# Performance work log

Measured on AMD Instinct MI355X. Metric: run time of the kernel, lower is better.

## Reference

```python
import jax, jax.numpy as jnp
import numpy as np

BN_EPS = 1e-5


def setup_inputs() -> dict:
    key = jax.random.key(0)
    ks = jax.random.split(key, 3)
    B, S, C, H, W = 4, 8, 64, 96, 96
    P = 6
    DIM = 768
    x = jax.random.normal(ks[0], (B, S, C, H, W), dtype=jnp.float32)
    conv_w = jax.random.normal(ks[1], (C, C, 3, 3), dtype=jnp.float32) * 0.05
    conv_b = jnp.zeros((C,), dtype=jnp.float32)
    bn_gamma = jnp.ones((C,), dtype=jnp.float32)
    bn_beta = jnp.zeros((C,), dtype=jnp.float32)
    bn_mean = jnp.zeros((C,), dtype=jnp.float32)
    bn_var = jnp.ones((C,), dtype=jnp.float32)
    proj_w = jax.random.normal(ks[2], (DIM, P * P * C), dtype=jnp.float32) * 0.02
    proj_b = jnp.zeros((DIM,), dtype=jnp.float32)
    mask = jnp.ones((P, P), dtype=jnp.float32)
    return {"x": x, "conv_w": conv_w, "conv_b": conv_b,
            "bn_gamma": bn_gamma, "bn_beta": bn_beta,
            "bn_mean": bn_mean, "bn_var": bn_var,
            "proj_w": proj_w, "proj_b": proj_b,
            "mask": mask, "patch_size": P}


def reference(x, conv_w, conv_b, bn_gamma, bn_beta, bn_mean, bn_var,
              proj_w, proj_b, mask, patch_size):
    B, S, C, H, W = x.shape
    p = patch_size
    Cout = conv_w.shape[0]
    # Fuse the per-frame loop: run conv over all B*S frames at once.
    xf = x.reshape(B * S, C, H, W)
    y = jax.lax.conv_general_dilated(
        xf, conv_w, window_strides=(1, 1), padding=[(1, 1), (1, 1)],
        dimension_numbers=("NCHW", "OIHW", "NCHW"))
    y = y + conv_b[None, :, None, None]
    # BatchNorm2d (eval-mode running stats); Dropout2d is identity at eval.
    inv = jax.lax.rsqrt(bn_var + BN_EPS)
    y = (y - bn_mean[None, :, None, None]) * (bn_gamma * inv)[None, :, None, None] \
        + bn_beta[None, :, None, None]
    y = jax.nn.gelu(y, approximate=False)  # torch GELU default = exact erf
    y = y.reshape(B, S, Cout, H, W)
    # Patch extraction, row-major over (l_idx, r_idx) exactly as the loop.
    pr = H // p  # patches per row
    patches = y.reshape(B, S, Cout, pr, p, pr, p).transpose(0, 1, 3, 5, 2, 4, 6)
    patches = patches.reshape(B, S, pr * pr, Cout, p, p) * mask  # [B,S,P,C,p,p]
    # Flatten(start_dim=2 on [B,S,C,p,p]) + Linear + GELU, batched over patches.
    flat = patches.reshape(B, S, pr * pr, Cout * p * p)
    tokens = jax.nn.gelu(
        jnp.einsum("bsnf,df->bsnd", flat, proj_w) + proj_b, approximate=False)
    return tokens, patches
```

## Files before the change

### kernel.cpp

```cpp
#include <hip/hip_runtime.h>
#include <hip/hip_bf16.h>
#include <math.h>


typedef unsigned short u16;
typedef __bf16 bf16x8 __attribute__((ext_vector_type(8)));
typedef float f32x4 __attribute__((ext_vector_type(4)));

#define NFRM 32
#define CH 64
#define HW 96
#define HWP 98
#define KP 2304
#define DIMN 768
#define MTOK 8192
#define TOKN (MTOK * DIMN)
#define NPAT (MTOK * KP)
#define XHWC_ELEMS ((size_t)NFRM * HWP * HWP * CH)
#define BP_OFF XHWC_ELEMS
#define PW_OFF (BP_OFF + 36864)
#define BSTR 200

static __device__ __forceinline__ u16 f2b(float f) {
  unsigned u = __builtin_bit_cast(unsigned, f);
  u += 0x7fffu + ((u >> 16) & 1u);
  return (u16)(u >> 16);
}
static __device__ __forceinline__ float gelu_f(float x) {
  return 0.5f * x * (1.0f + erff(x * 0.7071067811865476f));
}

typedef __attribute__((address_space(3))) unsigned int lds_uint;
typedef __attribute__((address_space(1))) const unsigned int g_uint;
static __device__ __forceinline__ void gload16(const u16* g, u16* s) {
  __builtin_amdgcn_global_load_lds((g_uint*)g, (lds_uint*)s, 16, 0, 0);
}

__global__ __launch_bounds__(256) void k_transpose(const float* __restrict__ x,
                                                   u16* __restrict__ xhwc) {
  __shared__ u16 tile[96 * 66];
  const int f = blockIdx.x / 96, h = blockIdx.x % 96;
  const int t = threadIdx.x;
  const float* xp = x + (size_t)f * CH * HW * HW + (size_t)h * HW;
#pragma unroll
  for (int k = 0; k < 6; ++k) {
    int e = (k * 256 + t) * 4;
    int ci = e / 96, w = e % 96;
    float4 v = *(const float4*)(xp + (size_t)ci * (HW * HW) + w);
    tile[(w + 0) * 66 + ci] = f2b(v.x);
    tile[(w + 1) * 66 + ci] = f2b(v.y);
    tile[(w + 2) * 66 + ci] = f2b(v.z);
    tile[(w + 3) * 66 + ci] = f2b(v.w);
  }
  __syncthreads();
  u16* op = xhwc + ((size_t)(f * HWP + h + 1) * HWP + 1) * CH;
#pragma unroll
  for (int k = 0; k < 12; ++k) {
    int e2 = (k * 256 + t) * 2;
    int w = e2 >> 6, ci = e2 & 63;
    *(unsigned*)(op + e2) = *(const unsigned*)(&tile[w * 66 + ci]);
  }
}

__global__ __launch_bounds__(256) void k_bpack(const float* __restrict__ w,
                                               u16* __restrict__ bp) {
  int e = blockIdx.x * 256 + threadIdx.x;
  int co = e / 576, r = e - co * 576, tap = r >> 6, ci = r & 63;
  bp[e] = f2b(w[(co * 64 + ci) * 9 + tap]);
}

__global__ __launch_bounds__(256) void k_pw(const float* __restrict__ pw,
                                            u16* __restrict__ dst) {
  int e = (blockIdx.x * 256 + threadIdx.x) * 4;
  float4 v = *(const float4*)(pw + e);
  ushort4 o;
  o.x = f2b(v.x); o.y = f2b(v.y); o.z = f2b(v.z); o.w = f2b(v.w);
  *(ushort4*)(dst + e) = o;
}

__global__ __launch_bounds__(256, 2) void k_conv(
    const u16* __restrict__ xhwc, const u16* __restrict__ bw,
    const float* __restrict__ cb, const float* __restrict__ gma,
    const float* __restrict__ bta, const float* __restrict__ mu,
    const float* __restrict__ var, const float* __restrict__ msk,
    float* __restrict__ pout) {
  __shared__ alignas(16) char SMEM[76800];
  u16* Asm = (u16*)SMEM;
  u16* Bsm = (u16*)(SMEM + 51200);
  float* Fsm = (float*)SMEM;

  const int bx = blockIdx.x;
  const int f = bx >> 5, rem = bx & 31, pr = rem >> 1, half = rem & 1;
  const int t = threadIdx.x, wv = t >> 6, l = t & 63, quad = l >> 4, lm = l & 15;
  const int wm = wv >> 1, wn = wv & 1;

  const u16* sbase = xhwc + (((size_t)f * HWP + pr * 6) * HWP + half * 48) * CH;
  const int pc = l >> 3;
  const int gsw = (l & 7) ^ pc;
  for (int c = wv; c < 50; c += 4) {
    const int p = c * 8 + pc;
    const int row = p / 50, ac = p - row * 50;
    gload16(sbase + ((size_t)row * HWP + ac) * CH + gsw * 8, Asm + c * 512);
  }

  int pb[9];
#pragma unroll
  for (int mf = 0; mf < 9; ++mf) {
    const int i16 = wm * 9 + mf;
    pb[mf] = (i16 / 3) * 50 + (i16 % 3) * 16 + lm;
  }
  f32x4 acc[9][2];
#pragma unroll
  for (int mf = 0; mf < 9; ++mf) {
    acc[mf][0] = (f32x4){0.f, 0.f, 0.f, 0.f};
    acc[mf][1] = (f32x4){0.f, 0.f, 0.f, 0.f};
  }

#pragma unroll
  for (int ph = 0; ph < 3; ++ph) {
    if (ph > 0) __syncthreads();
    for (int e = t; e < 1536; e += 256) {
      const int co = e / 24, kk = e - co * 24;
      *(uint4*)&Bsm[co * BSTR + kk * 8] =
          *(const uint4*)&bw[co * 576 + ph * 192 + kk * 8];
    }
    __syncthreads();
#pragma unroll
    for (int tp = 0; tp < 3; ++tp) {
      const int di = ph, dj = tp;
#pragma unroll
      for (int ks = 0; ks < 2; ++ks) {
        const int kq = ks * 4 + quad;
        const bf16x8 b0 = *(const bf16x8*)&Bsm[(wn * 32 + lm) * BSTR + tp * 64 + ks * 32 + quad * 8];
        const bf16x8 b1 = *(const bf16x8*)&Bsm[(wn * 32 + 16 + lm) * BSTR + tp * 64 + ks * 32 + quad * 8];
#pragma unroll
        for (int mf = 0; mf < 9; ++mf) {
          const int p = pb[mf] + di * 50 + dj;
          const bf16x8 a = *(const bf16x8*)&Asm[p * 64 + ((kq ^ (p & 7)) << 3)];
          acc[mf][0] = __builtin_amdgcn_mfma_f32_16x16x32_bf16(a, b0, acc[mf][0], 0, 0, 0);
          acc[mf][1] = __builtin_amdgcn_mfma_f32_16x16x32_bf16(a, b1, acc[mf][1], 0, 0, 0);
        }
      }
    }
  }

  __syncthreads();
#pragma unroll
  for (int nf = 0; nf < 2; ++nf) {
    const int co = wn * 32 + nf * 16 + lm;
    const float scv = gma[co] * rsqrtf(var[co] + 1e-5f);
    const float b2v = (cb[co] - mu[co]) * scv + bta[co];
#pragma unroll
    for (int mf = 0; mf < 9; ++mf) {
#pragma unroll
      for (int rg = 0; rg < 4; ++rg) {
        const int sp = wm * 144 + mf * 16 + quad * 4 + rg;
        const int orow = sp / 48, oc = sp - orow * 48;
        const int nl = oc / 6, pj = oc - nl * 6;
        const int jj = orow * 6 + pj;
        float v = acc[mf][nf][rg] * scv + b2v;
        v = gelu_f(v) * msk[jj];
        Fsm[nl * 2304 + co * 36 + jj] = v;
      }
    }
  }
  __syncthreads();
  float* pbase = pout + (size_t)(f * 256 + pr * 16 + half * 8) * KP;
#pragma unroll
  for (int k = 0; k < 18; ++k) {
    const int li = t + k * 256;
    *(float4*)&pbase[li * 4] = *(const float4*)&Fsm[li * 4];
  }
}

__global__ __launch_bounds__(256) void k_cvt(const float* __restrict__ pat,
                                             u16* __restrict__ abf) {
  int e = (blockIdx.x * 256 + threadIdx.x) * 4;
  float4 v = *(const float4*)(pat + e);
  ushort4 o;
  o.x = f2b(v.x); o.y = f2b(v.y); o.z = f2b(v.z); o.w = f2b(v.w);
  *(ushort4*)(abf + e) = o;
}

__global__ __launch_bounds__(256) void k_gemm(const u16* __restrict__ A,
                                              const u16* __restrict__ Bt,
                                              const float* __restrict__ pb,
                                              float* __restrict__ out) {
  __shared__ alignas(16) u16 As[128 * 64];
  __shared__ alignas(16) u16 Bs[64 * 64];
  const int bn = blockIdx.x % 12, bm = blockIdx.x / 12;
  const int m0 = bm * 128, n0 = bn * 64;
  const int t = threadIdx.x, wv = t >> 6, l = t & 63, quad = l >> 4, lm = l & 15;
  const int pc = l >> 3;
  const int gsw = (l & 7) ^ pc;

  f32x4 acc[2][4];
#pragma unroll
  for (int s = 0; s < 2; ++s)
#pragma unroll
    for (int u = 0; u < 4; ++u) acc[s][u] = (f32x4){0.f, 0.f, 0.f, 0.f};

  for (int k0 = 0; k0 < KP; k0 += 64) {
    __syncthreads();
    for (int c = wv; c < 24; c += 4) {
      if (c < 16) {
        const int row = c * 8 + pc;
        gload16(A + (size_t)(m0 + row) * KP + k0 + gsw * 8, As + c * 512);
      } else {
        const int row = (c - 16) * 8 + pc;
        gload16(Bt + (size_t)(n0 + row) * KP + k0 + gsw * 8, Bs + (c - 16) * 512);
      }
    }
    __syncthreads();
#pragma unroll
    for (int ks = 0; ks < 2; ++ks) {
      const int gx = ((ks * 4 + quad) ^ (lm & 7)) << 3;
      const bf16x8 a0 = *(const bf16x8*)&As[(wv * 32 + lm) * 64 + gx];
      const bf16x8 a1 = *(const bf16x8*)&As[(wv * 32 + 16 + lm) * 64 + gx];
#pragma unroll
      for (int u = 0; u < 4; ++u) {
        const bf16x8 b = *(const bf16x8*)&Bs[(u * 16 + lm) * 64 + gx];
        acc[0][u] = __builtin_amdgcn_mfma_f32_16x16x32_bf16(a0, b, acc[0][u], 0, 0, 0);
        acc[1][u] = __builtin_amdgcn_mfma_f32_16x16x32_bf16(a1, b, acc[1][u], 0, 0, 0);
      }
    }
  }
#pragma unroll
  for (int u = 0; u < 4; ++u) {
    const int n = n0 + u * 16 + lm;
    const float bias = pb[n];
#pragma unroll
    for (int s = 0; s < 2; ++s) {
#pragma unroll
      for (int rg = 0; rg < 4; ++rg) {
        const int m = m0 + wv * 32 + s * 16 + quad * 4 + rg;
        out[(size_t)m * DIMN + n] = gelu_f(acc[s][u][rg] + bias);
      }
    }
  }
}

extern "C" void kernel_launch(void* const* d_in, const int* in_sizes, int n_in,
                              void* d_out, int out_size, void* d_ws, size_t ws_size,
                              hipStream_t stream) {
  const float* x = (const float*)d_in[0];
  const float* conv_w = (const float*)d_in[1];
  const float* conv_b = (const float*)d_in[2];
  const float* bn_gamma = (const float*)d_in[3];
  const float* bn_beta = (const float*)d_in[4];
  const float* bn_mean = (const float*)d_in[5];
  const float* bn_var = (const float*)d_in[6];
  const float* proj_w = (const float*)d_in[7];
  const float* proj_b = (const float*)d_in[8];
  const float* mask = (const float*)d_in[9];
  float* out = (float*)d_out;
  float* patches = out + TOKN;
  u16* ws = (u16*)d_ws;
  u16* xhwc = ws;
  u16* bp = ws + BP_OFF;
  u16* pw = ws + PW_OFF;

  hipMemsetAsync(d_ws, 0, XHWC_ELEMS * sizeof(u16), stream);
  k_transpose<<<NFRM * HW, 256, 0, stream>>>(x, xhwc);
  k_bpack<<<144, 256, 0, stream>>>(conv_w, bp);
  k_pw<<<1728, 256, 0, stream>>>(proj_w, pw);
  k_conv<<<NFRM * 32, 256, 0, stream>>>(xhwc, bp, conv_b, bn_gamma, bn_beta,
                                        bn_mean, bn_var, mask, patches);
  k_cvt<<<18432, 256, 0, stream>>>(patches, xhwc);
  k_gemm<<<64 * 12, 256, 0, stream>>>(xhwc, pw, proj_b, out);
}
```

Before: 320.4 us.

## Fuse bf16 conversion into conv epilogue, stream weights from registers, widen GEMM K-tile

The conv kernel now writes a bf16 copy of the patches alongside the fp32 output, which removes the separate conversion pass over the large patch tensor whenever the workspace is large enough. Conv weights are read straight from global memory into registers with one-tap-ahead prefetch instead of being staged through LDS. That shrinks LDS enough to allow three blocks per CU, and the epilogue is split into two passes. A small halo-zeroing kernel replaces the full workspace memset, and both kernels remap block IDs for locality. The GEMM K-tile grows from 64 to 128 with a 16-way swizzle, halving the number of sync rounds while doubling LDS use.

```diff
diff --git a/kernel.cpp b/kernel.cpp
--- a/kernel.cpp
+++ b/kernel.cpp
@@ -19,7 +19,8 @@
 #define XHWC_ELEMS ((size_t)NFRM * HWP * HWP * CH)
 #define BP_OFF XHWC_ELEMS
 #define PW_OFF (BP_OFF + 36864)
-#define BSTR 200
+#define ABF_OFF (PW_OFF + 1769472)
+#define WS_NEED_FUSED (((size_t)ABF_OFF + (size_t)NPAT) * 2)
 
 static __device__ __forceinline__ u16 f2b(float f) {
   unsigned u = __builtin_bit_cast(unsigned, f);
@@ -34,6 +35,19 @@
 typedef __attribute__((address_space(1))) const unsigned int g_uint;
 static __device__ __forceinline__ void gload16(const u16* g, u16* s) {
   __builtin_amdgcn_global_load_lds((g_uint*)g, (lds_uint*)s, 16, 0, 0);
+}
+
+__global__ __launch_bounds__(256) void k_halo(u16* __restrict__ xhwc) {
+  const int e = blockIdx.x * 256 + threadIdx.x;
+  const int g = e & 7;
+  const int rest = e >> 3;
+  const int p = rest % 388, f = rest / 388;
+  int r, c;
+  if (p < 98)       { r = 0;       c = p; }
+  else if (p < 196) { r = 97;      c = p - 98; }
+  else if (p < 292) { r = p - 195; c = 0; }
+  else              { r = p - 291; c = 97; }
+  *(uint4*)&xhwc[(((size_t)f * HWP + r) * HWP + c) * CH + g * 8] = (uint4){0, 0, 0, 0};
 }
 
 __global__ __launch_bounds__(256) void k_transpose(const float* __restrict__ x,
@@ -78,19 +92,19 @@
   *(ushort4*)(dst + e) = o;
 }
 
-__global__ __launch_bounds__(256, 2) void k_conv(
+__global__ __launch_bounds__(256, 3) void k_conv(
     const u16* __restrict__ xhwc, const u16* __restrict__ bw,
     const float* __restrict__ cb, const float* __restrict__ gma,
     const float* __restrict__ bta, const float* __restrict__ mu,
     const float* __restrict__ var, const float* __restrict__ msk,
-    float* __restrict__ pout) {
-  __shared__ alignas(16) char SMEM[76800];
+    float* __restrict__ pout, u16* __restrict__ abf) {
+  __shared__ alignas(16) char SMEM[51200];
   u16* Asm = (u16*)SMEM;
-  u16* Bsm = (u16*)(SMEM + 51200);
   float* Fsm = (float*)SMEM;
 
-  const int bx = blockIdx.x;
-  const int f = bx >> 5, rem = bx & 31, pr = rem >> 1, half = rem & 1;
+  const int bid = blockIdx.x;
+  const int logical = (bid & 7) * 128 + (bid >> 3);
+  const int f = logical >> 5, rem = logical & 31, pr = rem >> 1, half = rem & 1;
   const int t = threadIdx.x, wv = t >> 6, l = t & 63, quad = l >> 4, lm = l & 15;
   const int wm = wv >> 1, wn = wv & 1;
 
@@ -116,35 +130,41 @@
     acc[mf][1] = (f32x4){0.f, 0.f, 0.f, 0.f};
   }
 
-#pragma unroll
-  for (int ph = 0; ph < 3; ++ph) {
-    if (ph > 0) __syncthreads();
-    for (int e = t; e < 1536; e += 256) {
-      const int co = e / 24, kk = e - co * 24;
-      *(uint4*)&Bsm[co * BSTR + kk * 8] =
-          *(const uint4*)&bw[co * 576 + ph * 192 + kk * 8];
-    }
-    __syncthreads();
-#pragma unroll
-    for (int tp = 0; tp < 3; ++tp) {
-      const int di = ph, dj = tp;
+  const u16* b0p = bw + (wn * 32 + lm) * 576 + quad * 8;
+  const u16* b1p = bw + (wn * 32 + 16 + lm) * 576 + quad * 8;
+  bf16x8 bc0[2], bc1[2], bn0[2], bn1[2];
+#pragma unroll
+  for (int ks = 0; ks < 2; ++ks) {
+    bc0[ks] = *(const bf16x8*)(b0p + ks * 32);
+    bc1[ks] = *(const bf16x8*)(b1p + ks * 32);
+  }
+  __syncthreads();
+
+#pragma unroll
+  for (int tap = 0; tap < 9; ++tap) {
+    const int di = tap / 3, dj = tap - di * 3;
+    if (tap < 8) {
 #pragma unroll
       for (int ks = 0; ks < 2; ++ks) {
-        const int kq = ks * 4 + quad;
-        const bf16x8 b0 = *(const bf16x8*)&Bsm[(wn * 32 + lm) * BSTR + tp * 64 + ks * 32 + quad * 8];
-        const bf16x8 b1 = *(const bf16x8*)&Bsm[(wn * 32 + 16 + lm) * BSTR + tp * 64 + ks * 32 + quad * 8];
-#pragma unroll
-        for (int mf = 0; mf < 9; ++mf) {
-          const int p = pb[mf] + di * 50 + dj;
-          const bf16x8 a = *(const bf16x8*)&Asm[p * 64 + ((kq ^ (p & 7)) << 3)];
-          acc[mf][0] = __builtin_amdgcn_mfma_f32_16x16x32_bf16(a, b0, acc[mf][0], 0, 0, 0);
-          acc[mf][1] = __builtin_amdgcn_mfma_f32_16x16x32_bf16(a, b1, acc[mf][1], 0, 0, 0);
-        }
-      }
-    }
-  }
-
-  __syncthreads();
+        bn0[ks] = *(const bf16x8*)(b0p + (tap + 1) * 64 + ks * 32);
+        bn1[ks] = *(const bf16x8*)(b1p + (tap + 1) * 64 + ks * 32);
+      }
+    }
+#pragma unroll
+    for (int ks = 0; ks < 2; ++ks) {
+      const int kq = ks * 4 + quad;
+#pragma unroll
+      for (int mf = 0; mf < 9; ++mf) {
+        const int p = pb[mf] + di * 50 + dj;
+        const bf16x8 a = *(const bf16x8*)&Asm[p * 64 + ((kq ^ (p & 7)) << 3)];
+        acc[mf][0] = __builtin_amdgcn_mfma_f32_16x16x32_bf16(a, bc0[ks], acc[mf][0], 0, 0, 0);
+        acc[mf][1] = __builtin_amdgcn_mfma_f32_16x16x32_bf16(a, bc1[ks], acc[mf][1], 0, 0, 0);
+      }
+    }
+#pragma unroll
+    for (int ks = 0; ks < 2; ++ks) { bc0[ks] = bn0[ks]; bc1[ks] = bn1[ks]; }
+  }
+
 #pragma unroll
   for (int nf = 0; nf < 2; ++nf) {
     const int co = wn * 32 + nf * 16 + lm;
@@ -152,24 +172,51 @@
     const float b2v = (cb[co] - mu[co]) * scv + bta[co];
 #pragma unroll
     for (int mf = 0; mf < 9; ++mf) {
+      const int orow = wm * 3 + mf / 3;
 #pragma unroll
       for (int rg = 0; rg < 4; ++rg) {
-        const int sp = wm * 144 + mf * 16 + quad * 4 + rg;
-        const int orow = sp / 48, oc = sp - orow * 48;
+        const int oc = (mf % 3) * 16 + quad * 4 + rg;
         const int nl = oc / 6, pj = oc - nl * 6;
         const int jj = orow * 6 + pj;
         float v = acc[mf][nf][rg] * scv + b2v;
-        v = gelu_f(v) * msk[jj];
-        Fsm[nl * 2304 + co * 36 + jj] = v;
+        acc[mf][nf][rg] = gelu_f(v) * msk[jj];
       }
     }
   }
   __syncthreads();
-  float* pbase = pout + (size_t)(f * 256 + pr * 16 + half * 8) * KP;
-#pragma unroll
-  for (int k = 0; k < 18; ++k) {
-    const int li = t + k * 256;
-    *(float4*)&pbase[li * 4] = *(const float4*)&Fsm[li * 4];
+#pragma unroll
+  for (int pass = 0; pass < 2; ++pass) {
+    if (pass) __syncthreads();
+#pragma unroll
+    for (int nf = 0; nf < 2; ++nf) {
+      const int co = wn * 32 + nf * 16 + lm;
+#pragma unroll
+      for (int mf = 0; mf < 9; ++mf) {
+        const int orow = wm * 3 + mf / 3;
+#pragma unroll
+        for (int rg = 0; rg < 4; ++rg) {
+          const int oc = (mf % 3) * 16 + quad * 4 + rg;
+          const int nl = oc / 6, pj = oc - nl * 6;
+          const int jj = orow * 6 + pj;
+          if ((nl >> 2) == pass)
+            Fsm[(nl & 3) * KP + co * 36 + jj] = acc[mf][nf][rg];
+        }
+      }
+    }
+    __syncthreads();
+    const size_t brow = (size_t)(f * 256 + pr * 16 + half * 8 + pass * 4) * KP;
+    float* pdst = pout + brow;
+#pragma unroll
+    for (int k = 0; k < 9; ++k) {
+      const int li = t + k * 256;
+      const float4 w = ((const float4*)Fsm)[li];
+      ((float4*)pdst)[li] = w;
+      if (abf) {
+        ushort4 o;
+        o.x = f2b(w.x); o.y = f2b(w.y); o.z = f2b(w.z); o.w = f2b(w.w);
+        *(ushort4*)&abf[brow + li * 4] = o;
+      }
+    }
   }
 }
 
@@ -186,13 +233,15 @@
                                               const u16* __restrict__ Bt,
                                               const float* __restrict__ pb,
                                               float* __restrict__ out) {
-  __shared__ alignas(16) u16 As[128 * 64];
-  __shared__ alignas(16) u16 Bs[64 * 64];
-  const int bn = blockIdx.x % 12, bm = blockIdx.x / 12;
+  __shared__ alignas(16) u16 As[128 * 128];
+  __shared__ alignas(16) u16 Bs[64 * 128];
+  const int bid = blockIdx.x;
+  const int logical = (bid & 7) * 96 + (bid >> 3);
+  const int bn = logical % 12, bm = logical / 12;
   const int m0 = bm * 128, n0 = bn * 64;
   const int t = threadIdx.x, wv = t >> 6, l = t & 63, quad = l >> 4, lm = l & 15;
-  const int pc = l >> 3;
-  const int gsw = (l & 7) ^ pc;
+  const int rl = l >> 4;
+  const int slot = l & 15;
 
   f32x4 acc[2][4];
 #pragma unroll
@@ -200,26 +249,28 @@
 #pragma unroll
     for (int u = 0; u < 4; ++u) acc[s][u] = (f32x4){0.f, 0.f, 0.f, 0.f};
 
-  for (int k0 = 0; k0 < KP; k0 += 64) {
+  for (int k0 = 0; k0 < KP; k0 += 128) {
     __syncthreads();
-    for (int c = wv; c < 24; c += 4) {
-      if (c < 16) {
-        const int row = c * 8 + pc;
+    for (int c = wv; c < 48; c += 4) {
+      if (c < 32) {
+        const int row = c * 4 + rl;
+        const int gsw = slot ^ (row & 15);
         gload16(A + (size_t)(m0 + row) * KP + k0 + gsw * 8, As + c * 512);
       } else {
-        const int row = (c - 16) * 8 + pc;
-        gload16(Bt + (size_t)(n0 + row) * KP + k0 + gsw * 8, Bs + (c - 16) * 512);
+        const int row = (c - 32) * 4 + rl;
+        const int gsw = slot ^ (row & 15);
+        gload16(Bt + (size_t)(n0 + row) * KP + k0 + gsw * 8, Bs + (c - 32) * 512);
       }
     }
     __syncthreads();
 #pragma unroll
-    for (int ks = 0; ks < 2; ++ks) {
-      const int gx = ((ks * 4 + quad) ^ (lm & 7)) << 3;
-      const bf16x8 a0 = *(const bf16x8*)&As[(wv * 32 + lm) * 64 + gx];
-      const bf16x8 a1 = *(const bf16x8*)&As[(wv * 32 + 16 + lm) * 64 + gx];
+    for (int ks = 0; ks < 4; ++ks) {
+      const int gx = ((ks * 4 + quad) ^ lm) << 3;
+      const bf16x8 a0 = *(const bf16x8*)&As[(wv * 32 + lm) * 128 + gx];
+      const bf16x8 a1 = *(const bf16x8*)&As[(wv * 32 + 16 + lm) * 128 + gx];
 #pragma unroll
       for (int u = 0; u < 4; ++u) {
-        const bf16x8 b = *(const bf16x8*)&Bs[(u * 16 + lm) * 64 + gx];
+        const bf16x8 b = *(const bf16x8*)&Bs[(u * 16 + lm) * 128 + gx];
         acc[0][u] = __builtin_amdgcn_mfma_f32_16x16x32_bf16(a0, b, acc[0][u], 0, 0, 0);
         acc[1][u] = __builtin_amdgcn_mfma_f32_16x16x32_bf16(a1, b, acc[1][u], 0, 0, 0);
       }
@@ -260,12 +311,18 @@
   u16* bp = ws + BP_OFF;
   u16* pw = ws + PW_OFF;
 
-  hipMemsetAsync(d_ws, 0, XHWC_ELEMS * sizeof(u16), stream);
+  const bool fused = ws_size >= WS_NEED_FUSED;
+  u16* abf = fused ? ws + ABF_OFF : (u16*)nullptr;
+
+  k_halo<<<388, 256, 0, stream>>>(xhwc);
   k_transpose<<<NFRM * HW, 256, 0, stream>>>(x, xhwc);
   k_bpack<<<144, 256, 0, stream>>>(conv_w, bp);
   k_pw<<<1728, 256, 0, stream>>>(proj_w, pw);
   k_conv<<<NFRM * 32, 256, 0, stream>>>(xhwc, bp, conv_b, bn_gamma, bn_beta,
-                                        bn_mean, bn_var, mask, patches);
-  k_cvt<<<18432, 256, 0, stream>>>(patches, xhwc);
-  k_gemm<<<64 * 12, 256, 0, stream>>>(xhwc, pw, proj_b, out);
-}
+                                        bn_mean, bn_var, mask, patches, abf);
+  if (!fused) {
+    k_cvt<<<18432, 256, 0, stream>>>(patches, xhwc);
+    abf = xhwc;
+  }
+  k_gemm<<<64 * 12, 256, 0, stream>>>(abf, pw, proj_b, out);
+}
```

Result: slower. 353.3 us (+10.3%).

## Fuse bf16 patch conversion into conv, zero only halo, rework GEMM staging

Applied to the files above, without the earlier changes.

The conv epilogue now also writes the bf16 copy of the patches into a dedicated workspace region when the workspace is large enough. This removes the separate fp32-to-bf16 conversion pass and its re-read of the patches tensor. The full-workspace memset is replaced by a small kernel that zeroes only the padding border of the HWC input. Separately, the projection GEMM switches from 64-wide async LDS loads with XOR swizzle to 32-wide K tiles loaded through registers into padded LDS rows. That doubles the number of barrier-synchronised iterations and drops the direct global-to-LDS path.

```diff
diff --git a/kernel.cpp b/kernel.cpp
--- a/kernel.cpp
+++ b/kernel.cpp
@@ -19,6 +19,8 @@
 #define XHWC_ELEMS ((size_t)NFRM * HWP * HWP * CH)
 #define BP_OFF XHWC_ELEMS
 #define PW_OFF (BP_OFF + 36864)
+#define ABF_OFF (PW_OFF + 1769472)
+#define WS_NEED_FUSED (((size_t)ABF_OFF + (size_t)NPAT) * 2)
 #define BSTR 200
 
 static __device__ __forceinline__ u16 f2b(float f) {
@@ -34,6 +36,19 @@
 typedef __attribute__((address_space(1))) const unsigned int g_uint;
 static __device__ __forceinline__ void gload16(const u16* g, u16* s) {
   __builtin_amdgcn_global_load_lds((g_uint*)g, (lds_uint*)s, 16, 0, 0);
+}
+
+__global__ __launch_bounds__(256) void k_halo(u16* __restrict__ xhwc) {
+  const int e = blockIdx.x * 256 + threadIdx.x;
+  const int g = e & 7;
+  const int rest = e >> 3;
+  const int p = rest % 388, f = rest / 388;
+  int r, c;
+  if (p < 98)       { r = 0;       c = p; }
+  else if (p < 196) { r = 97;      c = p - 98; }
+  else if (p < 292) { r = p - 195; c = 0; }
+  else              { r = p - 291; c = 97; }
+  *(uint4*)&xhwc[(((size_t)f * HWP + r) * HWP + c) * CH + g * 8] = (uint4){0, 0, 0, 0};
 }
 
 __global__ __launch_bounds__(256) void k_transpose(const float* __restrict__ x,
@@ -83,7 +98,7 @@
     const float* __restrict__ cb, const float* __restrict__ gma,
     const float* __restrict__ bta, const float* __restrict__ mu,
     const float* __restrict__ var, const float* __restrict__ msk,
-    float* __restrict__ pout) {
+    float* __restrict__ pout, u16* __restrict__ abf) {
   __shared__ alignas(16) char SMEM[76800];
   u16* Asm = (u16*)SMEM;
   u16* Bsm = (u16*)(SMEM + 51200);
@@ -165,11 +180,18 @@
     }
   }
   __syncthreads();
-  float* pbase = pout + (size_t)(f * 256 + pr * 16 + half * 8) * KP;
+  const size_t brow = (size_t)(f * 256 + pr * 16 + half * 8) * KP;
+  float* pbase = pout + brow;
 #pragma unroll
   for (int k = 0; k < 18; ++k) {
     const int li = t + k * 256;
-    *(float4*)&pbase[li * 4] = *(const float4*)&Fsm[li * 4];
+    const float4 w = *(const float4*)&Fsm[li * 4];
+    *(float4*)&pbase[li * 4] = w;
+    if (abf) {
+      ushort4 o;
+      o.x = f2b(w.x); o.y = f2b(w.y); o.z = f2b(w.z); o.w = f2b(w.w);
+      *(ushort4*)&abf[brow + li * 4] = o;
+    }
   }
 }
 
@@ -186,13 +208,12 @@
                                               const u16* __restrict__ Bt,
                                               const float* __restrict__ pb,
                                               float* __restrict__ out) {
-  __shared__ alignas(16) u16 As[128 * 64];
-  __shared__ alignas(16) u16 Bs[64 * 64];
+  __shared__ u16 As[128 * 40];
+  __shared__ u16 Bs[64 * 40];
   const int bn = blockIdx.x % 12, bm = blockIdx.x / 12;
   const int m0 = bm * 128, n0 = bn * 64;
   const int t = threadIdx.x, wv = t >> 6, l = t & 63, quad = l >> 4, lm = l & 15;
-  const int pc = l >> 3;
-  const int gsw = (l & 7) ^ pc;
+  const int ar = t >> 2, ac = (t & 3) * 8;
 
   f32x4 acc[2][4];
 #pragma unroll
@@ -200,29 +221,21 @@
 #pragma unroll
     for (int u = 0; u < 4; ++u) acc[s][u] = (f32x4){0.f, 0.f, 0.f, 0.f};
 
-  for (int k0 = 0; k0 < KP; k0 += 64) {
+  for (int k0 = 0; k0 < KP; k0 += 32) {
     __syncthreads();
-    for (int c = wv; c < 24; c += 4) {
-      if (c < 16) {
-        const int row = c * 8 + pc;
-        gload16(A + (size_t)(m0 + row) * KP + k0 + gsw * 8, As + c * 512);
-      } else {
-        const int row = (c - 16) * 8 + pc;
-        gload16(Bt + (size_t)(n0 + row) * KP + k0 + gsw * 8, Bs + (c - 16) * 512);
-      }
-    }
+    *(uint4*)&As[ar * 40 + ac] = *(const uint4*)&A[(size_t)(m0 + ar) * KP + k0 + ac];
+    *(uint4*)&As[(ar + 64) * 40 + ac] =
+        *(const uint4*)&A[(size_t)(m0 + ar + 64) * KP + k0 + ac];
+    *(uint4*)&Bs[ar * 40 + ac] = *(const uint4*)&Bt[(size_t)(n0 + ar) * KP + k0 + ac];
     __syncthreads();
-#pragma unroll
-    for (int ks = 0; ks < 2; ++ks) {
-      const int gx = ((ks * 4 + quad) ^ (lm & 7)) << 3;
-      const bf16x8 a0 = *(const bf16x8*)&As[(wv * 32 + lm) * 64 + gx];
-      const bf16x8 a1 = *(const bf16x8*)&As[(wv * 32 + 16 + lm) * 64 + gx];
-#pragma unroll
-      for (int u = 0; u < 4; ++u) {
-        const bf16x8 b = *(const bf16x8*)&Bs[(u * 16 + lm) * 64 + gx];
-        acc[0][u] = __builtin_amdgcn_mfma_f32_16x16x32_bf16(a0, b, acc[0][u], 0, 0, 0);
-        acc[1][u] = __builtin_amdgcn_mfma_f32_16x16x32_bf16(a1, b, acc[1][u], 0, 0, 0);
-      }
+    const int ko = quad * 8;
+    bf16x8 a0 = *(const bf16x8*)&As[(wv * 32 + lm) * 40 + ko];
+    bf16x8 a1 = *(const bf16x8*)&As[(wv * 32 + 16 + lm) * 40 + ko];
+#pragma unroll
+    for (int u = 0; u < 4; ++u) {
+      bf16x8 b = *(const bf16x8*)&Bs[(u * 16 + lm) * 40 + ko];
+      acc[0][u] = __builtin_amdgcn_mfma_f32_16x16x32_bf16(a0, b, acc[0][u], 0, 0, 0);
+      acc[1][u] = __builtin_amdgcn_mfma_f32_16x16x32_bf16(a1, b, acc[1][u], 0, 0, 0);
     }
   }
 #pragma unroll
@@ -260,12 +273,18 @@
   u16* bp = ws + BP_OFF;
   u16* pw = ws + PW_OFF;
 
-  hipMemsetAsync(d_ws, 0, XHWC_ELEMS * sizeof(u16), stream);
+  const bool fused = ws_size >= WS_NEED_FUSED;
+  u16* abf = fused ? ws + ABF_OFF : (u16*)nullptr;
+
+  k_halo<<<388, 256, 0, stream>>>(xhwc);
   k_transpose<<<NFRM * HW, 256, 0, stream>>>(x, xhwc);
   k_bpack<<<144, 256, 0, stream>>>(conv_w, bp);
   k_pw<<<1728, 256, 0, stream>>>(proj_w, pw);
   k_conv<<<NFRM * 32, 256, 0, stream>>>(xhwc, bp, conv_b, bn_gamma, bn_beta,
-                                        bn_mean, bn_var, mask, patches);
-  k_cvt<<<18432, 256, 0, stream>>>(patches, xhwc);
-  k_gemm<<<64 * 12, 256, 0, stream>>>(xhwc, pw, proj_b, out);
-}
+                                        bn_mean, bn_var, mask, patches, abf);
+  if (!fused) {
+    k_cvt<<<18432, 256, 0, stream>>>(patches, xhwc);
+    abf = xhwc;
+  }
+  k_gemm<<<64 * 12, 256, 0, stream>>>(abf, pw, proj_b, out);
+}
```

Result: no change. 322.8 us (+0.8%).
